# Performance work log

Hardware: AMD Instinct MI355X
Metric: run time of the kernel (lower is better)

Reference implementation:

```python
import jax, jax.numpy as jnp
import numpy as np

N_NODES = 50000
N_EDGES = 800000
D = 128          # embedding_dim
G = 3            # group_size
K = 4            # window_size
ALPHA = -0.5
WEIGHTS = (1.0, 1.0, 7.81, 45.28)
EPS = 1e-12      # torch F.normalize clamp_min


def _striped_projection(key):
    """Striped sparse random projection, densified (matches torch coalesce+to_dense)."""
    num_groups = D // G  # 42; columns 126..127 remain zero, as in the original
    k_off, k_sign = jax.random.split(key)
    row_idx = jnp.repeat(jnp.arange(N_NODES), num_groups)
    base = jnp.tile(jnp.arange(0, num_groups * G, G), N_NODES)
    off = jax.random.randint(k_off, (N_NODES * num_groups,), 0, G)
    col_idx = base + off
    scale = float(np.sqrt(G))  # 1/sqrt(density), density = 1/g
    vals = (jax.random.randint(k_sign, (N_NODES * num_groups,), 0, 2).astype(jnp.float32) * 2.0 - 1.0) * scale
    return jnp.zeros((N_NODES, D), jnp.float32).at[row_idx, col_idx].add(vals)


def setup_inputs() -> dict:
    key = jax.random.key(0)
    k1, k2, k3 = jax.random.split(key, 3)
    edge_row = jax.random.randint(k1, (N_EDGES,), 0, N_NODES)
    edge_col = jax.random.randint(k2, (N_EDGES,), 0, N_NODES)
    edge_val = jnp.ones((N_EDGES,), jnp.float32)
    R = _striped_projection(k3)
    return {"edge_row": edge_row, "edge_col": edge_col, "edge_val": edge_val, "R": R}


def reference(edge_row, edge_col, edge_val, R):
    N = R.shape[0]
    # degrees = row sums of sparse adjacency; zeros -> 1
    deg = jax.ops.segment_sum(edge_val, edge_row, num_segments=N)
    deg = jnp.where(deg == 0, 1.0, deg)
    # initial degree scaling: N_curr = R * deg**alpha
    x = R * (deg ** ALPHA)[:, None]
    inv_deg = (1.0 / deg)[:, None]
    acc = jnp.zeros_like(R)
    for i in range(K):
        # SpMM: out[r] = sum_{e: row[e]==r} val[e] * x[col[e]]
        x = jax.ops.segment_sum(edge_val[:, None] * x[edge_col], edge_row, num_segments=N)
        x = x * inv_deg  # transition-matrix ('trans') scaling
        nrm = jnp.maximum(jnp.sqrt(jnp.sum(x * x, axis=1, keepdims=True)), EPS)
        acc = acc + (x / nrm) * WEIGHTS[i]
    mean = acc.mean(axis=0)
    std = jnp.std(acc, axis=0, ddof=1)  # torch .std() is unbiased
    std = jnp.where(std == 0, 1.0, std)
    return (acc - mean) / std
```

## Files before the change

### kernel.cpp

```cpp
#include <hip/hip_runtime.h>
#include <math.h>

#define NN 50000
#define NE 800000
#define DD 128
#define NBKT 196
#define BCAP 5120
#define CHUNK 2048
#define NCHUNK ((NE + CHUNK - 1) / CHUNK)
#define CS1_NBLK 1024
#define CS_ROWS 49

static __device__ __forceinline__ float blo(unsigned int p) { return __uint_as_float(p << 16); }
static __device__ __forceinline__ float bhi(unsigned int p) { return __uint_as_float(p & 0xffff0000u); }
static __device__ __forceinline__ unsigned int pack2bf(float a, float b) {
    unsigned int ua = __float_as_uint(a);
    unsigned int ub = __float_as_uint(b);
    ua = ua + 0x7FFFu + ((ua >> 16) & 1u);
    ub = ub + 0x7FFFu + ((ub >> 16) & 1u);
    return (ua >> 16) | (ub & 0xffff0000u);
}

static __global__ __launch_bounds__(256) void bin_kernel(
    const int* __restrict__ erow, const int* __restrict__ ecol, const float* __restrict__ eval_,
    int* __restrict__ bucket_cursor, uint2* __restrict__ binned) {
    __shared__ uint2 sorted[CHUNK];
    __shared__ unsigned short sbin[CHUNK];
    __shared__ int hist[NBKT];
    __shared__ int bstart[NBKT];
    __shared__ int bcur[NBKT];
    __shared__ int gbase[NBKT];
    __shared__ int tmp[256];

    int t = threadIdx.x;
    int cbase = blockIdx.x * CHUNK;
    int cn = NE - cbase; if (cn > CHUNK) cn = CHUNK;

    for (int i = t; i < NBKT; i += 256) hist[i] = 0;
    __syncthreads();

    unsigned int rc[8]; unsigned int vv[8]; int bb[8];
    int nloc = 0;
    for (int i = t; i < cn; i += 256) {
        int g = cbase + i;
        int r = erow[g];
        int c = ecol[g];
        float v = eval_[g];
        rc[nloc] = (unsigned)r | ((unsigned)c << 16);
        vv[nloc] = __float_as_uint(v);
        int b = r >> 8;
        bb[nloc] = b;
        atomicAdd(&hist[b], 1);
        ++nloc;
    }
    __syncthreads();

    int hv = (t < NBKT) ? hist[t] : 0;
    tmp[t] = hv;
    __syncthreads();
    for (int off = 1; off < 256; off <<= 1) {
        int u = (t >= off) ? tmp[t - off] : 0;
        __syncthreads();
        tmp[t] += u;
        __syncthreads();
    }
    if (t < NBKT) {
        int ex = tmp[t] - hv;
        bstart[t] = ex;
        bcur[t] = ex;
        gbase[t] = atomicAdd(&bucket_cursor[t], hv);
    }
    __syncthreads();

    for (int k = 0; k < nloc; ++k) {
        int pos = atomicAdd(&bcur[bb[k]], 1);
        sorted[pos] = make_uint2(rc[k], vv[k]);
        sbin[pos] = (unsigned short)bb[k];
    }
    __syncthreads();

    for (int i = t; i < cn; i += 256) {
        int b = sbin[i];
        binned[(size_t)b * BCAP + gbase[b] + (i - bstart[b])] = sorted[i];
    }
}

static __global__ void bucket_scan_kernel(const int* __restrict__ bucket_cursor,
                                          int* __restrict__ bucket_base) {
    __shared__ int tmp[256];
    int t = threadIdx.x;
    int v = (t < NBKT) ? bucket_cursor[t] : 0;
    tmp[t] = v;
    __syncthreads();
    for (int off = 1; off < 256; off <<= 1) {
        int u = (t >= off) ? tmp[t - off] : 0;
        __syncthreads();
        tmp[t] += u;
        __syncthreads();
    }
    if (t < NBKT) bucket_base[t] = tmp[t] - v;
}

static __global__ __launch_bounds__(256) void sort_kernel(
    const uint2* __restrict__ binned, const int* __restrict__ bucket_cursor,
    const int* __restrict__ bucket_base, uint2* __restrict__ csr, int* __restrict__ row_start) {
    __shared__ uint2 buf[BCAP];
    __shared__ int hist[256];
    __shared__ int rcur[256];
    int b = blockIdx.x;
    int t = threadIdx.x;
    int cnt = bucket_cursor[b];
    int gb = bucket_base[b];
    int lo = b << 8;

    hist[t] = 0;
    __syncthreads();
    for (int i = t; i < cnt; i += 256) {
        uint2 e = binned[(size_t)b * BCAP + i];
        buf[i] = e;
        atomicAdd(&hist[(e.x & 0xFFFFu) - lo], 1);
    }
    __syncthreads();
    int hv = hist[t];
    rcur[t] = hv;
    __syncthreads();
    for (int off = 1; off < 256; off <<= 1) {
        int u = (t >= off) ? rcur[t - off] : 0;
        __syncthreads();
        rcur[t] += u;
        __syncthreads();
    }
    int excl = rcur[t] - hv;
    int r = lo + t;
    if (r < NN) row_start[r] = gb + excl;
    if (b == NBKT - 1 && t == 255) row_start[NN] = gb + cnt;
    rcur[t] = excl;
    __syncthreads();
    for (int i = t; i < cnt; i += 256) {
        uint2 e = buf[i];
        int rr = (int)(e.x & 0xFFFFu) - lo;
        int pos = atomicAdd(&rcur[rr], 1);
        csr[(size_t)gb + pos] = make_uint2(e.x >> 16, e.y);
    }
}

static __global__ void deg_from_csr_kernel(const int* __restrict__ row_start,
                                           const uint2* __restrict__ csr,
                                           float* __restrict__ deg, int n) {
    int r = blockIdx.x * blockDim.x + threadIdx.x;
    if (r < n) {
        int s = row_start[r], e = row_start[r + 1];
        float sum = 0.0f;
        for (int j = s; j < e; ++j) sum += __uint_as_float(csr[j].y);
        deg[r] = (sum == 0.0f) ? 1.0f : sum;
    }
}

static __global__ void init_x_kernel(const float* __restrict__ R, const float* __restrict__ deg,
                                     unsigned int* __restrict__ xq, int npairs) {
    int i = blockIdx.x * blockDim.x + threadIdx.x;
    if (i < npairs) {
        float d = deg[i >> 6];
        float sc = rsqrtf(d);
        float a = R[2 * i] * sc;
        float b = R[2 * i + 1] * sc;
        xq[i] = pack2bf(a, b);
    }
}

static __global__ __launch_bounds__(256) void spmm_fused_kernel(
    const int* __restrict__ row_start, const uint2* __restrict__ csr,
    const uint2* __restrict__ x2, const float* __restrict__ deg,
    uint2* __restrict__ x_next2, float* __restrict__ acc, float weight, int overwrite) {
    int wave = threadIdx.x >> 6;
    int lane = threadIdx.x & 63;
    int half = lane >> 5;
    int sub  = lane & 31;
    int row = blockIdx.x * 4 + wave;
    int s = row_start[row];
    int e = row_start[row + 1];

    float a0 = 0.f, a1 = 0.f, a2 = 0.f, a3 = 0.f;
    for (int base = s; base < e; base += 64) {
        int j = base + lane;
        int cl = 0;
        float vl = 0.0f;
        if (j < e) { uint2 t2 = csr[j]; cl = (int)t2.x; vl = __uint_as_float(t2.y); }
        int cnt = e - base; if (cnt > 64) cnt = 64;
        int k = 0;
        for (; k + 8 <= cnt; k += 8) {
            int c0 = __shfl(cl, k + half);
            int c1 = __shfl(cl, k + 2 + half);
            int c2 = __shfl(cl, k + 4 + half);
            int c3 = __shfl(cl, k + 6 + half);
            float v0 = __shfl(vl, k + half);
            float v1 = __shfl(vl, k + 2 + half);
            float v2 = __shfl(vl, k + 4 + half);
            float v3 = __shfl(vl, k + 6 + half);
            uint2 p0 = x2[(size_t)c0 * 32 + sub];
            uint2 p1 = x2[(size_t)c1 * 32 + sub];
            uint2 p2 = x2[(size_t)c2 * 32 + sub];
            uint2 p3 = x2[(size_t)c3 * 32 + sub];
            a0 += v0 * blo(p0.x); a1 += v0 * bhi(p0.x); a2 += v0 * blo(p0.y); a3 += v0 * bhi(p0.y);
            a0 += v1 * blo(p1.x); a1 += v1 * bhi(p1.x); a2 += v1 * blo(p1.y); a3 += v1 * bhi(p1.y);
            a0 += v2 * blo(p2.x); a1 += v2 * bhi(p2.x); a2 += v2 * blo(p2.y); a3 += v2 * bhi(p2.y);
            a0 += v3 * blo(p3.x); a1 += v3 * bhi(p3.x); a2 += v3 * blo(p3.y); a3 += v3 * bhi(p3.y);
        }
        for (; k < cnt; k += 2) {
            int kk = k + half;
            int c = __shfl(cl, kk);
            float v = __shfl(vl, kk);
            uint2 p = x2[(size_t)c * 32 + sub];
            a0 += v * blo(p.x); a1 += v * bhi(p.x); a2 += v * blo(p.y); a3 += v * bhi(p.y);
        }
    }
    a0 += __shfl_xor(a0, 32);
    a1 += __shfl_xor(a1, 32);
    a2 += __shfl_xor(a2, 32);
    a3 += __shfl_xor(a3, 32);

    float id = 1.0f / deg[row];
    a0 *= id; a1 *= id; a2 *= id; a3 *= id;

    float ss = a0 * a0 + a1 * a1 + a2 * a2 + a3 * a3;
#pragma unroll
    for (int m = 1; m <= 16; m <<= 1) ss += __shfl_xor(ss, m);
    float nrm = fmaxf(sqrtf(ss), 1e-12f);
    float w = weight / nrm;

    if (half == 0) {
        x_next2[(size_t)row * 32 + sub] = make_uint2(pack2bf(a0, a1), pack2bf(a2, a3));
        float4* acc4 = (float4*)acc;
        size_t idx = (size_t)row * 32 + sub;
        if (overwrite) {
            acc4[idx] = make_float4(a0 * w, a1 * w, a2 * w, a3 * w);
        } else {
            float4 p = acc4[idx];
            p.x += a0 * w; p.y += a1 * w; p.z += a2 * w; p.w += a3 * w;
            acc4[idx] = p;
        }
    }
}

static __global__ __launch_bounds__(256) void colstats_kernel(
    const float* __restrict__ acc, double* __restrict__ psum, double* __restrict__ psumsq) {
    __shared__ double shs[4 * 64 * 2];
    __shared__ double shq[4 * 64 * 2];
    int t = threadIdx.x;
    int wv = t >> 6;
    int cp = t & 63;
    int rbeg = blockIdx.x * CS_ROWS;
    int rend = rbeg + CS_ROWS; if (rend > NN) rend = NN;

    const float2* __restrict__ acc2 = (const float2*)acc;
    double s0 = 0.0, q0 = 0.0, s1 = 0.0, q1 = 0.0;
    for (int r = rbeg + wv; r < rend; r += 4) {
        float2 v = acc2[(size_t)r * 64 + cp];
        s0 += (double)v.x; q0 += (double)v.x * (double)v.x;
        s1 += (double)v.y; q1 += (double)v.y * (double)v.y;
    }
    shs[(wv * 64 + cp) * 2 + 0] = s0;
    shs[(wv * 64 + cp) * 2 + 1] = s1;
    shq[(wv * 64 + cp) * 2 + 0] = q0;
    shq[(wv * 64 + cp) * 2 + 1] = q1;
    __syncthreads();
    if (t < 128) {
        double s = shs[t] + shs[128 + t] + shs[256 + t] + shs[384 + t];
        double q = shq[t] + shq[128 + t] + shq[256 + t] + shq[384 + t];
        int col = (t >> 1) * 2 + (t & 1);
        psum[(size_t)blockIdx.x * DD + col] = s;
        psumsq[(size_t)blockIdx.x * DD + col] = q;
    }
}

static __global__ __launch_bounds__(256) void colstats_fold_kernel(
    const double* __restrict__ psum, const double* __restrict__ psumsq,
    float* __restrict__ mean, float* __restrict__ invstd) {
    __shared__ double ss[256], qq[256];
    int c = blockIdx.x;
    int t = threadIdx.x;
    double s = 0.0, q = 0.0;
    for (int b = t; b < CS1_NBLK; b += 256) {
        s += psum[(size_t)b * DD + c];
        q += psumsq[(size_t)b * DD + c];
    }
    ss[t] = s; qq[t] = q;
    __syncthreads();
    for (int off = 128; off > 0; off >>= 1) {
        if (t < off) { ss[t] += ss[t + off]; qq[t] += qq[t + off]; }
        __syncthreads();
    }
    if (t == 0) {
        double m = ss[0] / (double)NN;
        double var = (qq[0] - (double)NN * m * m) / (double)(NN - 1);
        if (var < 0.0) var = 0.0;
        double sd = sqrt(var);
        if (sd == 0.0) sd = 1.0;
        mean[c] = (float)m;
        invstd[c] = (float)(1.0 / sd);
    }
}

static __global__ void normalize_kernel(float* __restrict__ out, const float* __restrict__ mean,
                                        const float* __restrict__ invstd, int total) {
    int i = blockIdx.x * blockDim.x + threadIdx.x;
    if (i < total) {
        int c = i & 127;
        out[i] = (out[i] - mean[c]) * invstd[c];
    }
}

extern "C" void kernel_launch(void* const* d_in, const int* in_sizes, int n_in,
                              void* d_out, int out_size, void* d_ws, size_t ws_size,
                              hipStream_t stream) {
    const int* erow = (const int*)d_in[0];
    const int* ecol = (const int*)d_in[1];
    const float* eval_ = (const float*)d_in[2];
    const float* R = (const float*)d_in[3];
    float* out = (float*)d_out;

    char* ws = (char*)d_ws;
    size_t off = 0;
    auto alloc = [&](size_t bytes) -> char* {
        char* p = ws + off;
        off += (bytes + 255) & ~(size_t)255;
        return p;
    };
    float* deg          = (float*)alloc(NN * sizeof(float));
    int* bucket_cursor  = (int*)alloc(NBKT * sizeof(int));
    int* bucket_base    = (int*)alloc(NBKT * sizeof(int));
    int* row_start      = (int*)alloc((NN + 1) * sizeof(int));
    uint2* binned       = (uint2*)alloc((size_t)NBKT * BCAP * sizeof(uint2));
    uint2* csr          = (uint2*)alloc((size_t)NE * sizeof(uint2));
    uint2* x_a          = (uint2*)alloc((size_t)NN * 32 * sizeof(uint2));
    uint2* x_b          = (uint2*)alloc((size_t)NN * 32 * sizeof(uint2));
    double* psum        = (double*)alloc((size_t)CS1_NBLK * DD * sizeof(double));
    double* psumsq      = (double*)alloc((size_t)CS1_NBLK * DD * sizeof(double));
    float* meanbuf      = (float*)alloc(DD * sizeof(float));
    float* invstdb      = (float*)alloc(DD * sizeof(float));

    hipMemsetAsync(bucket_cursor, 0, NBKT * sizeof(int), stream);

    const int total = NN * DD;
    const int npairs = total / 2;

    bin_kernel<<<NCHUNK, 256, 0, stream>>>(erow, ecol, eval_, bucket_cursor, binned);
    bucket_scan_kernel<<<1, 256, 0, stream>>>(bucket_cursor, bucket_base);
    sort_kernel<<<NBKT, 256, 0, stream>>>(binned, bucket_cursor, bucket_base, csr, row_start);

    deg_from_csr_kernel<<<(NN + 255) / 256, 256, 0, stream>>>(row_start, csr, deg, NN);
    init_x_kernel<<<(npairs + 255) / 256, 256, 0, stream>>>(R, deg, (unsigned int*)x_a, npairs);

    const float weights[4] = {1.0f, 1.0f, 7.81f, 45.28f};
    uint2* xs[2] = {x_a, x_b};
    for (int i = 0; i < 4; ++i) {
        spmm_fused_kernel<<<NN / 4, 256, 0, stream>>>(row_start, csr,
                                                      xs[i & 1], deg, xs[(i + 1) & 1],
                                                      out, weights[i], i == 0 ? 1 : 0);
    }

    colstats_kernel<<<CS1_NBLK, 256, 0, stream>>>(out, psum, psumsq);
    colstats_fold_kernel<<<DD, 256, 0, stream>>>(psum, psumsq, meanbuf, invstdb);
    normalize_kernel<<<(total + 255) / 256, 256, 0, stream>>>(out, meanbuf, invstdb, total);
}
```

Before: 295.7 us.

## Defer fp32 accumulator into combine-stats pass and widen SpMM gathers to 16 bytes

```diff
diff --git a/kernel.cpp b/kernel.cpp
--- a/kernel.cpp
+++ b/kernel.cpp
@@ -157,30 +157,32 @@
 }
 
 static __global__ void init_x_kernel(const float* __restrict__ R, const float* __restrict__ deg,
-                                     unsigned int* __restrict__ xq, int npairs) {
+                                     uint4* __restrict__ xq, int nquads) {
     int i = blockIdx.x * blockDim.x + threadIdx.x;
-    if (i < npairs) {
-        float d = deg[i >> 6];
+    if (i < nquads) {
+        float d = deg[i >> 4];
         float sc = rsqrtf(d);
-        float a = R[2 * i] * sc;
-        float b = R[2 * i + 1] * sc;
-        xq[i] = pack2bf(a, b);
+        const float4* R4 = (const float4*)R;
+        float4 f0 = R4[i * 2];
+        float4 f1 = R4[i * 2 + 1];
+        xq[i] = make_uint4(pack2bf(f0.x * sc, f0.y * sc), pack2bf(f0.z * sc, f0.w * sc),
+                           pack2bf(f1.x * sc, f1.y * sc), pack2bf(f1.z * sc, f1.w * sc));
     }
 }
 
 static __global__ __launch_bounds__(256) void spmm_fused_kernel(
     const int* __restrict__ row_start, const uint2* __restrict__ csr,
-    const uint2* __restrict__ x2, const float* __restrict__ deg,
-    uint2* __restrict__ x_next2, float* __restrict__ acc, float weight, int overwrite) {
+    const uint4* __restrict__ x4, const float* __restrict__ deg,
+    uint4* __restrict__ x_next4, float* __restrict__ s_out, float weight) {
     int wave = threadIdx.x >> 6;
     int lane = threadIdx.x & 63;
-    int half = lane >> 5;
-    int sub  = lane & 31;
+    int quarter = lane >> 4;
+    int sub = lane & 15;
     int row = blockIdx.x * 4 + wave;
     int s = row_start[row];
     int e = row_start[row + 1];
 
-    float a0 = 0.f, a1 = 0.f, a2 = 0.f, a3 = 0.f;
+    float a0 = 0.f, a1 = 0.f, a2 = 0.f, a3 = 0.f, a4 = 0.f, a5 = 0.f, a6 = 0.f, a7 = 0.f;
     for (int base = s; base < e; base += 64) {
         int j = base + lane;
         int cl = 0;
@@ -189,87 +191,96 @@
         int cnt = e - base; if (cnt > 64) cnt = 64;
         int k = 0;
         for (; k + 8 <= cnt; k += 8) {
-            int c0 = __shfl(cl, k + half);
-            int c1 = __shfl(cl, k + 2 + half);
-            int c2 = __shfl(cl, k + 4 + half);
-            int c3 = __shfl(cl, k + 6 + half);
-            float v0 = __shfl(vl, k + half);
-            float v1 = __shfl(vl, k + 2 + half);
-            float v2 = __shfl(vl, k + 4 + half);
-            float v3 = __shfl(vl, k + 6 + half);
-            uint2 p0 = x2[(size_t)c0 * 32 + sub];
-            uint2 p1 = x2[(size_t)c1 * 32 + sub];
-            uint2 p2 = x2[(size_t)c2 * 32 + sub];
-            uint2 p3 = x2[(size_t)c3 * 32 + sub];
-            a0 += v0 * blo(p0.x); a1 += v0 * bhi(p0.x); a2 += v0 * blo(p0.y); a3 += v0 * bhi(p0.y);
-            a0 += v1 * blo(p1.x); a1 += v1 * bhi(p1.x); a2 += v1 * blo(p1.y); a3 += v1 * bhi(p1.y);
-            a0 += v2 * blo(p2.x); a1 += v2 * bhi(p2.x); a2 += v2 * blo(p2.y); a3 += v2 * bhi(p2.y);
-            a0 += v3 * blo(p3.x); a1 += v3 * bhi(p3.x); a2 += v3 * blo(p3.y); a3 += v3 * bhi(p3.y);
+            int ca = __shfl(cl, k + quarter);
+            int cb = __shfl(cl, k + 4 + quarter);
+            float va = __shfl(vl, k + quarter);
+            float vb = __shfl(vl, k + 4 + quarter);
+            uint4 pa = x4[(size_t)ca * 16 + sub];
+            uint4 pb = x4[(size_t)cb * 16 + sub];
+            a0 += va * blo(pa.x); a1 += va * bhi(pa.x); a2 += va * blo(pa.y); a3 += va * bhi(pa.y);
+            a4 += va * blo(pa.z); a5 += va * bhi(pa.z); a6 += va * blo(pa.w); a7 += va * bhi(pa.w);
+            a0 += vb * blo(pb.x); a1 += vb * bhi(pb.x); a2 += vb * blo(pb.y); a3 += vb * bhi(pb.y);
+            a4 += vb * blo(pb.z); a5 += vb * bhi(pb.z); a6 += vb * blo(pb.w); a7 += vb * bhi(pb.w);
         }
-        for (; k < cnt; k += 2) {
-            int kk = k + half;
+        for (; k < cnt; k += 4) {
+            int kk = k + quarter;
             int c = __shfl(cl, kk);
             float v = __shfl(vl, kk);
-            uint2 p = x2[(size_t)c * 32 + sub];
+            uint4 p = x4[(size_t)c * 16 + sub];
             a0 += v * blo(p.x); a1 += v * bhi(p.x); a2 += v * blo(p.y); a3 += v * bhi(p.y);
+            a4 += v * blo(p.z); a5 += v * bhi(p.z); a6 += v * blo(p.w); a7 += v * bhi(p.w);
         }
     }
-    a0 += __shfl_xor(a0, 32);
-    a1 += __shfl_xor(a1, 32);
-    a2 += __shfl_xor(a2, 32);
-    a3 += __shfl_xor(a3, 32);
+    a0 += __shfl_xor(a0, 16); a1 += __shfl_xor(a1, 16); a2 += __shfl_xor(a2, 16); a3 += __shfl_xor(a3, 16);
+    a4 += __shfl_xor(a4, 16); a5 += __shfl_xor(a5, 16); a6 += __shfl_xor(a6, 16); a7 += __shfl_xor(a7, 16);
+    a0 += __shfl_xor(a0, 32); a1 += __shfl_xor(a1, 32); a2 += __shfl_xor(a2, 32); a3 += __shfl_xor(a3, 32);
+    a4 += __shfl_xor(a4, 32); a5 += __shfl_xor(a5, 32); a6 += __shfl_xor(a6, 32); a7 += __shfl_xor(a7, 32);
 
     float id = 1.0f / deg[row];
-    a0 *= id; a1 *= id; a2 *= id; a3 *= id;
-
-    float ss = a0 * a0 + a1 * a1 + a2 * a2 + a3 * a3;
+    a0 *= id; a1 *= id; a2 *= id; a3 *= id; a4 *= id; a5 *= id; a6 *= id; a7 *= id;
+
+    float ss = a0 * a0 + a1 * a1 + a2 * a2 + a3 * a3 + a4 * a4 + a5 * a5 + a6 * a6 + a7 * a7;
 #pragma unroll
-    for (int m = 1; m <= 16; m <<= 1) ss += __shfl_xor(ss, m);
+    for (int m = 1; m <= 8; m <<= 1) ss += __shfl_xor(ss, m);
     float nrm = fmaxf(sqrtf(ss), 1e-12f);
-    float w = weight / nrm;
-
-    if (half == 0) {
-        x_next2[(size_t)row * 32 + sub] = make_uint2(pack2bf(a0, a1), pack2bf(a2, a3));
-        float4* acc4 = (float4*)acc;
-        size_t idx = (size_t)row * 32 + sub;
-        if (overwrite) {
-            acc4[idx] = make_float4(a0 * w, a1 * w, a2 * w, a3 * w);
-        } else {
-            float4 p = acc4[idx];
-            p.x += a0 * w; p.y += a1 * w; p.z += a2 * w; p.w += a3 * w;
-            acc4[idx] = p;
-        }
-    }
-}
-
-static __global__ __launch_bounds__(256) void colstats_kernel(
-    const float* __restrict__ acc, double* __restrict__ psum, double* __restrict__ psumsq) {
-    __shared__ double shs[4 * 64 * 2];
-    __shared__ double shq[4 * 64 * 2];
-    int t = threadIdx.x;
-    int wv = t >> 6;
-    int cp = t & 63;
+
+    if (lane < 16) {
+        x_next4[(size_t)row * 16 + sub] = make_uint4(pack2bf(a0, a1), pack2bf(a2, a3),
+                                                     pack2bf(a4, a5), pack2bf(a6, a7));
+    }
+    if (lane == 0) s_out[row] = weight / nrm;
+}
+
+static __global__ __launch_bounds__(256) void combine_stats_kernel(
+    const uint4* __restrict__ x1, const uint4* __restrict__ x2,
+    const uint4* __restrict__ x3, const uint4* __restrict__ x4,
+    const float* __restrict__ s1, const float* __restrict__ s2,
+    const float* __restrict__ s3, const float* __restrict__ s4,
+    float* __restrict__ out, double* __restrict__ psum, double* __restrict__ psumsq) {
+    __shared__ double shs[256 * 8];
+    __shared__ double shq[256 * 8];
+    int t = threadIdx.x;
+    int sub = t & 15;
+    int ro = t >> 4;
     int rbeg = blockIdx.x * CS_ROWS;
     int rend = rbeg + CS_ROWS; if (rend > NN) rend = NN;
 
-    const float2* __restrict__ acc2 = (const float2*)acc;
-    double s0 = 0.0, q0 = 0.0, s1 = 0.0, q1 = 0.0;
-    for (int r = rbeg + wv; r < rend; r += 4) {
-        float2 v = acc2[(size_t)r * 64 + cp];
-        s0 += (double)v.x; q0 += (double)v.x * (double)v.x;
-        s1 += (double)v.y; q1 += (double)v.y * (double)v.y;
-    }
-    shs[(wv * 64 + cp) * 2 + 0] = s0;
-    shs[(wv * 64 + cp) * 2 + 1] = s1;
-    shq[(wv * 64 + cp) * 2 + 0] = q0;
-    shq[(wv * 64 + cp) * 2 + 1] = q1;
-    __syncthreads();
-    if (t < 128) {
-        double s = shs[t] + shs[128 + t] + shs[256 + t] + shs[384 + t];
-        double q = shq[t] + shq[128 + t] + shq[256 + t] + shq[384 + t];
-        int col = (t >> 1) * 2 + (t & 1);
-        psum[(size_t)blockIdx.x * DD + col] = s;
-        psumsq[(size_t)blockIdx.x * DD + col] = q;
+    double ls[8], lq[8];
+#pragma unroll
+    for (int j = 0; j < 8; ++j) { ls[j] = 0.0; lq[j] = 0.0; }
+
+    float4* out4 = (float4*)out;
+    for (int r = rbeg + ro; r < rend; r += 16) {
+        float w1 = s1[r], w2 = s2[r], w3 = s3[r], w4 = s4[r];
+        size_t xi = (size_t)r * 16 + sub;
+        uint4 q1 = x1[xi], q2 = x2[xi], q3 = x3[xi], q4 = x4[xi];
+        float v[8];
+        v[0] = w1 * blo(q1.x) + w2 * blo(q2.x) + w3 * blo(q3.x) + w4 * blo(q4.x);
+        v[1] = w1 * bhi(q1.x) + w2 * bhi(q2.x) + w3 * bhi(q3.x) + w4 * bhi(q4.x);
+        v[2] = w1 * blo(q1.y) + w2 * blo(q2.y) + w3 * blo(q3.y) + w4 * blo(q4.y);
+        v[3] = w1 * bhi(q1.y) + w2 * bhi(q2.y) + w3 * bhi(q3.y) + w4 * bhi(q4.y);
+        v[4] = w1 * blo(q1.z) + w2 * blo(q2.z) + w3 * blo(q3.z) + w4 * blo(q4.z);
+        v[5] = w1 * bhi(q1.z) + w2 * bhi(q2.z) + w3 * bhi(q3.z) + w4 * bhi(q4.z);
+        v[6] = w1 * blo(q1.w) + w2 * blo(q2.w) + w3 * blo(q3.w) + w4 * blo(q4.w);
+        v[7] = w1 * bhi(q1.w) + w2 * bhi(q2.w) + w3 * bhi(q3.w) + w4 * bhi(q4.w);
+        out4[(size_t)r * 32 + sub * 2]     = make_float4(v[0], v[1], v[2], v[3]);
+        out4[(size_t)r * 32 + sub * 2 + 1] = make_float4(v[4], v[5], v[6], v[7]);
+#pragma unroll
+        for (int j = 0; j < 8; ++j) { ls[j] += (double)v[j]; lq[j] += (double)v[j] * (double)v[j]; }
+    }
+#pragma unroll
+    for (int j = 0; j < 8; ++j) { shs[t * 8 + j] = ls[j]; shq[t * 8 + j] = lq[j]; }
+    __syncthreads();
+    if (t < DD) {
+        int cs = t >> 3, cj = t & 7;
+        double s = 0.0, q = 0.0;
+        for (int g = 0; g < 16; ++g) {
+            int src = (g * 16 + cs) * 8 + cj;
+            s += shs[src];
+            q += shq[src];
+        }
+        psum[(size_t)blockIdx.x * DD + t] = s;
+        psumsq[(size_t)blockIdx.x * DD + t] = q;
     }
 }
 
@@ -332,8 +343,15 @@
     int* row_start      = (int*)alloc((NN + 1) * sizeof(int));
     uint2* binned       = (uint2*)alloc((size_t)NBKT * BCAP * sizeof(uint2));
     uint2* csr          = (uint2*)alloc((size_t)NE * sizeof(uint2));
-    uint2* x_a          = (uint2*)alloc((size_t)NN * 32 * sizeof(uint2));
-    uint2* x_b          = (uint2*)alloc((size_t)NN * 32 * sizeof(uint2));
+    uint4* x0           = (uint4*)alloc((size_t)NN * 16 * sizeof(uint4));
+    uint4* x1           = (uint4*)alloc((size_t)NN * 16 * sizeof(uint4));
+    uint4* x2           = (uint4*)alloc((size_t)NN * 16 * sizeof(uint4));
+    uint4* x3           = (uint4*)alloc((size_t)NN * 16 * sizeof(uint4));
+    uint4* x4           = (uint4*)alloc((size_t)NN * 16 * sizeof(uint4));
+    float* s1           = (float*)alloc(NN * sizeof(float));
+    float* s2           = (float*)alloc(NN * sizeof(float));
+    float* s3           = (float*)alloc(NN * sizeof(float));
+    float* s4           = (float*)alloc(NN * sizeof(float));
     double* psum        = (double*)alloc((size_t)CS1_NBLK * DD * sizeof(double));
     double* psumsq      = (double*)alloc((size_t)CS1_NBLK * DD * sizeof(double));
     float* meanbuf      = (float*)alloc(DD * sizeof(float));
@@ -342,24 +360,22 @@
     hipMemsetAsync(bucket_cursor, 0, NBKT * sizeof(int), stream);
 
     const int total = NN * DD;
-    const int npairs = total / 2;
+    const int nquads = total / 8;
 
     bin_kernel<<<NCHUNK, 256, 0, stream>>>(erow, ecol, eval_, bucket_cursor, binned);
     bucket_scan_kernel<<<1, 256, 0, stream>>>(bucket_cursor, bucket_base);
     sort_kernel<<<NBKT, 256, 0, stream>>>(binned, bucket_cursor, bucket_base, csr, row_start);
 
     deg_from_csr_kernel<<<(NN + 255) / 256, 256, 0, stream>>>(row_start, csr, deg, NN);
-    init_x_kernel<<<(npairs + 255) / 256, 256, 0, stream>>>(R, deg, (unsigned int*)x_a, npairs);
-
-    const float weights[4] = {1.0f, 1.0f, 7.81f, 45.28f};
-    uint2* xs[2] = {x_a, x_b};
-    for (int i = 0; i < 4; ++i) {
-        spmm_fused_kernel<<<NN / 4, 256, 0, stream>>>(row_start, csr,
-                                                      xs[i & 1], deg, xs[(i + 1) & 1],
-                                                      out, weights[i], i == 0 ? 1 : 0);
-    }
-
-    colstats_kernel<<<CS1_NBLK, 256, 0, stream>>>(out, psum, psumsq);
+    init_x_kernel<<<(nquads + 255) / 256, 256, 0, stream>>>(R, deg, x0, nquads);
+
+    spmm_fused_kernel<<<NN / 4, 256, 0, stream>>>(row_start, csr, x0, deg, x1, s1, 1.0f);
+    spmm_fused_kernel<<<NN / 4, 256, 0, stream>>>(row_start, csr, x1, deg, x2, s2, 1.0f);
+    spmm_fused_kernel<<<NN / 4, 256, 0, stream>>>(row_start, csr, x2, deg, x3, s3, 7.81f);
+    spmm_fused_kernel<<<NN / 4, 256, 0, stream>>>(row_start, csr, x3, deg, x4, s4, 45.28f);
+
+    combine_stats_kernel<<<CS1_NBLK, 256, 0, stream>>>(x1, x2, x3, x4, s1, s2, s3, s4,
+                                                       out, psum, psumsq);
     colstats_fold_kernel<<<DD, 256, 0, stream>>>(psum, psumsq, meanbuf, invstdb);
     normalize_kernel<<<(total + 255) / 256, 256, 0, stream>>>(out, meanbuf, invstdb, total);
 }
```

Result: faster. 273.7 us (-7.5%).
